# Optimization experiments

Measured on AMD Instinct MI355X. Metric: run time of the kernel, lower is better.

## Reference

```python
import jax, jax.numpy as jnp
import numpy as np

N_NODES = 50000
N_EDGES = 800000
IN_F, H_F, OUT_F = 256, 256, 128


def setup_inputs() -> dict:
    key = jax.random.key(0)
    k1, k2, k3, k4, k5, k6 = jax.random.split(key, 6)
    in_feat = jax.random.normal(k1, (N_NODES, IN_F), dtype=jnp.float32)
    src = jax.random.randint(k2, (N_EDGES,), 0, N_NODES, dtype=jnp.int32)
    dst = jax.random.randint(k3, (N_EDGES,), 0, N_NODES, dtype=jnp.int32)
    s1 = 1.0 / np.sqrt(IN_F)
    s2 = 1.0 / np.sqrt(H_F)
    W1 = jax.random.uniform(k4, (IN_F, H_F), dtype=jnp.float32, minval=-s1, maxval=s1)
    b1 = jnp.zeros((H_F,), dtype=jnp.float32)
    W2 = jax.random.uniform(k5, (H_F, OUT_F), dtype=jnp.float32, minval=-s2, maxval=s2)
    b2 = jnp.zeros((OUT_F,), dtype=jnp.float32)
    return {"in_feat": in_feat, "src": src, "dst": dst,
            "W1": W1, "b1": b1, "W2": W2, "b2": b2}


def _graph_conv(x, W, b, src, dst, n_nodes):
    # DGL GraphConv with norm='both':
    #   h = D_in^{-1/2} A D_out^{-1/2} (X W) + b   (degrees clamped to min 1)
    ones = jnp.ones((src.shape[0],), dtype=x.dtype)
    deg_out = jax.ops.segment_sum(ones, src, num_segments=n_nodes)
    deg_in = jax.ops.segment_sum(ones, dst, num_segments=n_nodes)
    norm_out = jax.lax.rsqrt(jnp.maximum(deg_out, 1.0))  # [N]
    norm_in = jax.lax.rsqrt(jnp.maximum(deg_in, 1.0))    # [N]
    h = (x @ W) * norm_out[:, None]                       # [N, F_out]
    agg = jax.ops.segment_sum(h[src], dst, num_segments=n_nodes)  # SpMM
    return agg * norm_in[:, None] + b


def reference(in_feat, src, dst, W1, b1, W2, b2):
    n = in_feat.shape[0]
    h = _graph_conv(in_feat, W1, b1, src, dst, n)
    h = jax.nn.relu(h)
    h = _graph_conv(h, W2, b2, src, dst, n)
    # dgl.mean_nodes over a single graph -> mean across all nodes
    return jnp.mean(h, axis=0)  # [OUT_F]
```

## Files before the change

### kernel.cpp

```cpp
#include <hip/hip_runtime.h>


#define NNODES 50000
#define NEDGES 800000
#define DPAD   32
#define G1_BM   ((NNODES + 127) / 128)
#define MEGA_NB 3911
#define WS_NB   2048
#define NQUAD   (NNODES / 4)

typedef __bf16 bf16x8 __attribute__((ext_vector_type(8)));
typedef float f32x4 __attribute__((ext_vector_type(4)));
typedef float f32x2 __attribute__((ext_vector_type(2)));

__device__ __forceinline__ unsigned short f2b(float f) {
    union { float f; unsigned u; } v; v.f = f;
    unsigned r = 0x7fffu + ((v.u >> 16) & 1u);
    return (unsigned short)((v.u + r) >> 16);
}
__device__ __forceinline__ unsigned char f2fp8(float x) {
    return (unsigned char)(__builtin_amdgcn_cvt_pk_fp8_f32(x, x, 0, false) & 0xff);
}
__device__ __forceinline__ float rdeg(int d) {
    return __frsqrt_rn((float)max(d, 1));
}

__global__ void k_cast_w1(const float* __restrict__ W1, unsigned short* __restrict__ W1t,
                          uint4* __restrict__ deg0) {
    int id = blockIdx.x * blockDim.x + threadIdx.x;
    int k = id >> 8, n = id & 255;
    W1t[n * 256 + k] = f2b(W1[id]);
    const uint4 z = make_uint4(0, 0, 0, 0);
    for (int j = id; j < 2 * NNODES * DPAD / 4; j += 65536) deg0[j] = z;
}

__global__ __launch_bounds__(256) void k_mega1(
    const int* __restrict__ src, const int* __restrict__ dst,
    int* __restrict__ degOut, int* __restrict__ degIn,
    unsigned short* __restrict__ col2, unsigned short* __restrict__ dst2,
    const float* __restrict__ X, const unsigned short* __restrict__ W1t,
    unsigned char* __restrict__ H, int M) {
    __shared__ __align__(16) unsigned short As[128][40];
    __shared__ __align__(16) unsigned short Bs[128][40];

    int bid = blockIdx.x;
    int tid = threadIdx.x;

    if ((bid % 5) != 4) {
        int did = bid - (bid + 1) / 5;
        int e = did * 256 + tid;
        if (e < NEDGES) {
            int s = src[e], d = dst[e];
            int si = atomicAdd(&degIn[d * DPAD], 1);
            if (si < 64) col2[d * 64 + si] = (unsigned short)s;
            int so = atomicAdd(&degOut[s * DPAD], 1);
            if (so < 64) dst2[s * 64 + so] = (unsigned short)d;
        }
        return;
    }

    int g = bid / 5;
    int bm = g % G1_BM, bn = g / G1_BM;
    int m0 = bm * 128, n0 = bn * 128;
    int lane = tid & 63, wave = tid >> 6;
    int wm = (wave >> 1) * 64, wn = (wave & 1) * 64;
    int q = lane >> 4, r16 = lane & 15;

    f32x4 acc[4][4];
#pragma unroll
    for (int i = 0; i < 4; i++)
#pragma unroll
        for (int j = 0; j < 4; j++) acc[i][j] = 0.f;

    int c0 = tid, c1 = tid + 256;
    int r0 = c0 >> 2, k0c = (c0 & 3) * 8;
    int r1 = c1 >> 2, k1c = (c1 & 3) * 8;
    const float* Ar0 = X + (size_t)min(m0 + r0, M - 1) * 256;
    const float* Ar1 = X + (size_t)min(m0 + r1, M - 1) * 256;
    const unsigned short* Br0 = W1t + (size_t)(n0 + r0) * 256;
    const unsigned short* Br1 = W1t + (size_t)(n0 + r1) * 256;

    auto pk2u = [](float a, float b) -> unsigned {
        unsigned short x = f2b(a), y = f2b(b);
        return (unsigned)x | ((unsigned)y << 16);
    };

    for (int k0 = 0; k0 < 256; k0 += 32) {
        float4 fa0 = *(const float4*)(Ar0 + k0 + k0c);
        float4 fa1 = *(const float4*)(Ar0 + k0 + k0c + 4);
        float4 fb0 = *(const float4*)(Ar1 + k0 + k1c);
        float4 fb1 = *(const float4*)(Ar1 + k0 + k1c + 4);
        uint4 vb0 = *(const uint4*)(Br0 + k0 + k0c);
        uint4 vb1 = *(const uint4*)(Br1 + k0 + k1c);
        uint4 va0 = make_uint4(pk2u(fa0.x, fa0.y), pk2u(fa0.z, fa0.w), pk2u(fa1.x, fa1.y), pk2u(fa1.z, fa1.w));
        uint4 va1 = make_uint4(pk2u(fb0.x, fb0.y), pk2u(fb0.z, fb0.w), pk2u(fb1.x, fb1.y), pk2u(fb1.z, fb1.w));
        __syncthreads();
        *(uint4*)&As[r0][k0c] = va0;
        *(uint4*)&As[r1][k1c] = va1;
        *(uint4*)&Bs[r0][k0c] = vb0;
        *(uint4*)&Bs[r1][k1c] = vb1;
        __syncthreads();
        bf16x8 af[4], bf[4];
#pragma unroll
        for (int i = 0; i < 4; i++)
            af[i] = *(const bf16x8*)&As[wm + i * 16 + r16][q * 8];
#pragma unroll
        for (int j = 0; j < 4; j++)
            bf[j] = *(const bf16x8*)&Bs[wn + j * 16 + r16][q * 8];
#pragma unroll
        for (int i = 0; i < 4; i++)
#pragma unroll
            for (int j = 0; j < 4; j++)
                acc[i][j] = __builtin_amdgcn_mfma_f32_16x16x32_bf16(af[i], bf[j], acc[i][j], 0, 0, 0);
    }

#pragma unroll
    for (int i = 0; i < 4; i++) {
#pragma unroll
        for (int rr = 0; rr < 4; rr++) {
            int m = m0 + wm + i * 16 + q * 4 + rr;
            if (m < M) {
                unsigned char* Hp = H + (size_t)m * 256 + n0 + wn + r16;
#pragma unroll
                for (int j = 0; j < 4; j++)
                    Hp[j * 16] = f2fp8(acc[i][j][rr]);
            }
        }
    }
}

__global__ __launch_bounds__(256) void k_norms(
    const int* __restrict__ degOut, const int* __restrict__ degIn,
    float* __restrict__ normOut, float* __restrict__ normIn,
    int* __restrict__ degc) {
    int i = blockIdx.x * blockDim.x + threadIdx.x;
    if (i < NNODES) {
        int dI = degIn[i * DPAD], dO = degOut[i * DPAD];
        normIn[i] = rdeg(dI);
        normOut[i] = rdeg(dO);
        degc[i] = min(dI, 64) | (min(dO, 64) << 16);
    }
}

__global__ __launch_bounds__(256) void k_spmm_wsum(
    const unsigned char* __restrict__ H, const float* __restrict__ normIn,
    const float* __restrict__ normOut, const int* __restrict__ degc,
    const unsigned short* __restrict__ col2, const unsigned short* __restrict__ dst2,
    const float* __restrict__ bias, float* __restrict__ vpart) {
    __shared__ float sm[4][256];
    int wave = threadIdx.x >> 6;
    int lane = threadIdx.x & 63;
    int f = lane * 4;
    const unsigned char* Hf = H + f;
    float4 bv = *(const float4*)(bias + f);
    float vac0 = 0.f, vac1 = 0.f, vac2 = 0.f, vac3 = 0.f;

    int qd = blockIdx.x;
    int node = qd * 4 + wave;
    int pDC = 0, pc = 0, pd = 0;
    float pNI = 0.f, pNO = 0.f;
    if (qd < NQUAD) {
        pDC = degc[node]; pNI = normIn[node]; pNO = normOut[node];
        pc = (int)col2[(size_t)node * 64 + lane];
        pd = (int)dst2[(size_t)node * 64 + lane];
    }

    while (qd < NQUAD) {
        int dI = pDC & 0xffff, dO = pDC >> 16;
        float nI = pNI, nO = pNO;
        int myc = pc, myd = pd;

        int nqd = qd + gridDim.x;
        if (nqd < NQUAD) {
            int nn = nqd * 4 + wave;
            pDC = degc[nn]; pNI = normIn[nn]; pNO = normOut[nn];
            pc = (int)col2[(size_t)nn * 64 + lane];
            pd = (int)dst2[(size_t)nn * 64 + lane];
        }

        float sIn = 0.f;
        if (lane < dO) sIn = normIn[myd];
#pragma unroll
        for (int o = 32; o > 0; o >>= 1) sIn += __shfl_xor(sIn, o);
        float wn = nO * sIn;

        float a0 = 0.f, a1 = 0.f, a2 = 0.f, a3 = 0.f;
        int i = 0;
        for (; i + 16 <= dI; i += 16) {
            float w[16]; unsigned v[16];
#pragma unroll
            for (int u = 0; u < 16; u++) {
                int c = __builtin_amdgcn_readlane(myc, i + u);
                w[u] = normOut[c];
                v[u] = *(const unsigned*)(Hf + (size_t)c * 256);
            }
#pragma unroll
            for (int u = 0; u < 16; u++) {
                f32x2 lo = __builtin_amdgcn_cvt_pk_f32_fp8(v[u], false);
                f32x2 hi = __builtin_amdgcn_cvt_pk_f32_fp8(v[u], true);
                a0 += lo.x * w[u]; a1 += lo.y * w[u];
                a2 += hi.x * w[u]; a3 += hi.y * w[u];
            }
        }
        for (; i + 4 <= dI; i += 4) {
            float w[4]; unsigned v[4];
#pragma unroll
            for (int u = 0; u < 4; u++) {
                int c = __builtin_amdgcn_readlane(myc, i + u);
                w[u] = normOut[c];
                v[u] = *(const unsigned*)(Hf + (size_t)c * 256);
            }
#pragma unroll
            for (int u = 0; u < 4; u++) {
                f32x2 lo = __builtin_amdgcn_cvt_pk_f32_fp8(v[u], false);
                f32x2 hi = __builtin_amdgcn_cvt_pk_f32_fp8(v[u], true);
                a0 += lo.x * w[u]; a1 += lo.y * w[u];
                a2 += hi.x * w[u]; a3 += hi.y * w[u];
            }
        }
        for (; i < dI; i++) {
            int c = __builtin_amdgcn_readlane(myc, i);
            float w = normOut[c];
            unsigned v = *(const unsigned*)(Hf + (size_t)c * 256);
            f32x2 lo = __builtin_amdgcn_cvt_pk_f32_fp8(v, false);
            f32x2 hi = __builtin_amdgcn_cvt_pk_f32_fp8(v, true);
            a0 += lo.x * w; a1 += lo.y * w;
            a2 += hi.x * w; a3 += hi.y * w;
        }

        vac0 += wn * fmaxf(a0 * nI + bv.x, 0.f);
        vac1 += wn * fmaxf(a1 * nI + bv.y, 0.f);
        vac2 += wn * fmaxf(a2 * nI + bv.z, 0.f);
        vac3 += wn * fmaxf(a3 * nI + bv.w, 0.f);

        qd = nqd;
    }

    *(float4*)&sm[wave][f] = make_float4(vac0, vac1, vac2, vac3);
    __syncthreads();
    int t = threadIdx.x;
    float s4 = sm[0][t] + sm[1][t] + sm[2][t] + sm[3][t];
    vpart[(size_t)blockIdx.x * 256 + t] = s4;
}

__global__ __launch_bounds__(256) void k_red1(const float* __restrict__ vpart,
                                              float* __restrict__ vred) {
    int b = blockIdx.x;
    int t = threadIdx.x;
    float s = 0.f;
    for (int i = b; i < WS_NB; i += 64) s += vpart[(size_t)i * 256 + t];
    vred[(size_t)b * 256 + t] = s;
}

__global__ __launch_bounds__(1024) void k_final(
    const float* __restrict__ vred, const float* __restrict__ W2,
    const float* __restrict__ b2, float* __restrict__ out) {
    __shared__ float part[4][256];
    __shared__ float v[256];
    int t = threadIdx.x;
    int feat = t & 255, pr = t >> 8;
    float s = 0.f;
    for (int i = pr; i < 64; i += 4) s += vred[(size_t)i * 256 + feat];
    part[pr][feat] = s;
    __syncthreads();
    if (t < 256) v[t] = part[0][t] + part[1][t] + part[2][t] + part[3][t];
    __syncthreads();
    if (t < 128) {
        float o = 0.f;
        for (int k = 0; k < 256; k++) o += v[k] * W2[k * 128 + t];
        out[t] = o * (1.0f / (float)NNODES) + b2[t];
    }
}

extern "C" void kernel_launch(void* const* d_in, const int* in_sizes, int n_in,
                              void* d_out, int out_size, void* d_ws, size_t ws_size,
                              hipStream_t stream) {
    const float* X   = (const float*)d_in[0];
    const int*   src = (const int*)d_in[1];
    const int*   dst = (const int*)d_in[2];
    const float* W1  = (const float*)d_in[3];
    const float* b1  = (const float*)d_in[4];
    const float* W2  = (const float*)d_in[5];
    const float* b2  = (const float*)d_in[6];
    float* out = (float*)d_out;

    const int n = NNODES;

    char* p = (char*)d_ws;
    auto carve = [&](size_t bytes) -> void* {
        void* r = (void*)p;
        p += (bytes + 255) & ~(size_t)255;
        return r;
    };
    int*   degOut  = (int*)carve((size_t)2 * n * DPAD * sizeof(int));
    int*   degIn   = degOut + (size_t)n * DPAD;
    unsigned short* col2 = (unsigned short*)carve((size_t)n * 64 * 2);
    unsigned short* dst2 = (unsigned short*)carve((size_t)n * 64 * 2);
    unsigned short* W1t  = (unsigned short*)carve((size_t)256 * 256 * 2);
    unsigned char*  bufA = (unsigned char*)carve((size_t)n * 256);
    float* vpart  = (float*)carve((size_t)WS_NB * 256 * sizeof(float));
    float* vred   = (float*)carve((size_t)64 * 256 * sizeof(float));
    float* normOutD = (float*)carve((size_t)n * sizeof(float));
    float* normInD  = (float*)carve((size_t)n * sizeof(float));
    int*   degc     = (int*)carve((size_t)n * sizeof(int));

    k_cast_w1<<<256, 256, 0, stream>>>(W1, W1t, (uint4*)degOut);

    k_mega1<<<MEGA_NB, 256, 0, stream>>>(src, dst, degOut, degIn, col2, dst2, X, W1t, bufA, n);

    k_norms<<<(n + 255) / 256, 256, 0, stream>>>(degOut, degIn, normOutD, normInD, degc);

    k_spmm_wsum<<<WS_NB, 256, 0, stream>>>(bufA, normInD, normOutD, degc, col2, dst2, b1, vpart);

    k_red1<<<64, 256, 0, stream>>>(vpart, vred);
    k_final<<<1, 1024, 0, stream>>>(vred, W2, b2, out);
}
```

Measured before the change: 230.2 us.

## Replace out-degree CSR with LDS histograms for out-degree and weight sums

Drops the per-source adjacency (dst2) and padded out-degree atomics from the edge pass. A new histogram kernel computes out-degree and the per-source sum of normIn[dst] in shared-memory partial sums over edge chunks, and a merge kernel reduces them into norms and a precomputed weight per node. The SpMM kernel then reads that weight instead of gathering normIn over dst2 and doing a wave reduction. The cost is an extra full edge pass plus large partial-sum scratch traffic, in exchange for fewer global atomics and scattered writes. DegIn padding is also removed, so in-degree atomics now hit adjacent words.

```diff
diff --git a/kernel.cpp b/kernel.cpp
--- a/kernel.cpp
+++ b/kernel.cpp
@@ -3,11 +3,14 @@
 
 #define NNODES 50000
 #define NEDGES 800000
-#define DPAD   32
 #define G1_BM   ((NNODES + 127) / 128)
 #define MEGA_NB 3911
 #define WS_NB   2048
 #define NQUAD   (NNODES / 4)
+#define CH      64
+#define EPC     (NEDGES / CH)
+#define QN      12500
+#define HN      25000
 
 typedef __bf16 bf16x8 __attribute__((ext_vector_type(8)));
 typedef float f32x4 __attribute__((ext_vector_type(4)));
@@ -30,14 +33,12 @@
     int id = blockIdx.x * blockDim.x + threadIdx.x;
     int k = id >> 8, n = id & 255;
     W1t[n * 256 + k] = f2b(W1[id]);
-    const uint4 z = make_uint4(0, 0, 0, 0);
-    for (int j = id; j < 2 * NNODES * DPAD / 4; j += 65536) deg0[j] = z;
+    if (id < NNODES / 4) deg0[id] = make_uint4(0, 0, 0, 0);
 }
 
 __global__ __launch_bounds__(256) void k_mega1(
     const int* __restrict__ src, const int* __restrict__ dst,
-    int* __restrict__ degOut, int* __restrict__ degIn,
-    unsigned short* __restrict__ col2, unsigned short* __restrict__ dst2,
+    int* __restrict__ degIn, unsigned short* __restrict__ col2,
     const float* __restrict__ X, const unsigned short* __restrict__ W1t,
     unsigned char* __restrict__ H, int M) {
     __shared__ __align__(16) unsigned short As[128][40];
@@ -51,10 +52,8 @@
         int e = did * 256 + tid;
         if (e < NEDGES) {
             int s = src[e], d = dst[e];
-            int si = atomicAdd(&degIn[d * DPAD], 1);
+            int si = atomicAdd(&degIn[d], 1);
             if (si < 64) col2[d * 64 + si] = (unsigned short)s;
-            int so = atomicAdd(&degOut[s * DPAD], 1);
-            if (so < 64) dst2[s * 64 + so] = (unsigned short)d;
         }
         return;
     }
@@ -129,23 +128,77 @@
     }
 }
 
-__global__ __launch_bounds__(256) void k_norms(
-    const int* __restrict__ degOut, const int* __restrict__ degIn,
-    float* __restrict__ normOut, float* __restrict__ normIn,
-    int* __restrict__ degc) {
+__global__ __launch_bounds__(256) void k_hist(
+    const int* __restrict__ src, const int* __restrict__ dst,
+    const int* __restrict__ degIn,
+    float* __restrict__ wsumP,
+    unsigned* __restrict__ degOutP)
+{
+    __shared__ unsigned lds[QN];
+    int b = blockIdx.x, t = threadIdx.x;
+    for (int i = t; i < QN; i += 256) lds[i] = 0;
+    __syncthreads();
+
+    if (b < 256) {
+        int c = b >> 2, q = b & 3;
+        int base = c * EPC;
+        int lo = q * QN;
+        float* w = (float*)lds;
+        for (int e = base + t; e < base + EPC; e += 256) {
+            int s = src[e], d = dst[e];
+            unsigned r = (unsigned)(s - lo);
+            if (r < QN) {
+                float ni = rdeg(degIn[d]);
+                atomicAdd(&w[r], ni);
+            }
+        }
+        __syncthreads();
+        float* outp = wsumP + (size_t)b * QN;
+        for (int i = t; i < QN; i += 256) outp[i] = w[i];
+    } else {
+        int b2 = b - 256;
+        int c = b2 >> 1, h = b2 & 1;
+        int base = c * EPC;
+        int lo = h * HN;
+        for (int e = base + t; e < base + EPC; e += 256) {
+            unsigned r = (unsigned)(src[e] - lo);
+            if (r < HN) atomicAdd(&lds[r >> 1], 1u << ((r & 1) * 16));
+        }
+        __syncthreads();
+        unsigned* outp = degOutP + (size_t)b2 * QN;
+        for (int i = t; i < QN; i += 256) outp[i] = lds[i];
+    }
+}
+
+__global__ __launch_bounds__(256) void k_merge(
+    const float* __restrict__ wsumP, const unsigned* __restrict__ degOutP,
+    const int* __restrict__ degIn,
+    float* __restrict__ normIn, float* __restrict__ normOut,
+    float* __restrict__ wgt, int* __restrict__ degc) {
     int i = blockIdx.x * blockDim.x + threadIdx.x;
-    if (i < NNODES) {
-        int dI = degIn[i * DPAD], dO = degOut[i * DPAD];
-        normIn[i] = rdeg(dI);
-        normOut[i] = rdeg(dO);
-        degc[i] = min(dI, 64) | (min(dO, 64) << 16);
-    }
+    if (i >= NNODES) return;
+    int q = i / QN, li = i - q * QN;
+    float ws = 0.f;
+#pragma unroll 8
+    for (int c = 0; c < CH; c++) ws += wsumP[(size_t)(c * 4 + q) * QN + li];
+    int h = i / HN, r = i - h * HN;
+    int wd = r >> 1, sel = r & 1;
+    unsigned dsum = 0;
+#pragma unroll 8
+    for (int c = 0; c < CH; c++) dsum += degOutP[(size_t)(c * 2 + h) * QN + wd];
+    int dO = (int)((dsum >> (sel * 16)) & 0xffffu);
+    int dI = degIn[i];
+    float nI = rdeg(dI), nO = rdeg(dO);
+    normIn[i] = nI;
+    normOut[i] = nO;
+    wgt[i] = nO * ws;
+    degc[i] = min(dI, 64);
 }
 
 __global__ __launch_bounds__(256) void k_spmm_wsum(
     const unsigned char* __restrict__ H, const float* __restrict__ normIn,
-    const float* __restrict__ normOut, const int* __restrict__ degc,
-    const unsigned short* __restrict__ col2, const unsigned short* __restrict__ dst2,
+    const float* __restrict__ normOut, const float* __restrict__ wgt,
+    const int* __restrict__ degc, const unsigned short* __restrict__ col2,
     const float* __restrict__ bias, float* __restrict__ vpart) {
     __shared__ float sm[4][256];
     int wave = threadIdx.x >> 6;
@@ -157,32 +210,23 @@
 
     int qd = blockIdx.x;
     int node = qd * 4 + wave;
-    int pDC = 0, pc = 0, pd = 0;
-    float pNI = 0.f, pNO = 0.f;
+    int pDI = 0, pc = 0;
+    float pNI = 0.f, pW = 0.f;
     if (qd < NQUAD) {
-        pDC = degc[node]; pNI = normIn[node]; pNO = normOut[node];
+        pDI = degc[node]; pNI = normIn[node]; pW = wgt[node];
         pc = (int)col2[(size_t)node * 64 + lane];
-        pd = (int)dst2[(size_t)node * 64 + lane];
     }
 
     while (qd < NQUAD) {
-        int dI = pDC & 0xffff, dO = pDC >> 16;
-        float nI = pNI, nO = pNO;
-        int myc = pc, myd = pd;
+        int dI = pDI, myc = pc;
+        float nI = pNI, wn = pW;
 
         int nqd = qd + gridDim.x;
         if (nqd < NQUAD) {
             int nn = nqd * 4 + wave;
-            pDC = degc[nn]; pNI = normIn[nn]; pNO = normOut[nn];
+            pDI = degc[nn]; pNI = normIn[nn]; pW = wgt[nn];
             pc = (int)col2[(size_t)nn * 64 + lane];
-            pd = (int)dst2[(size_t)nn * 64 + lane];
-        }
-
-        float sIn = 0.f;
-        if (lane < dO) sIn = normIn[myd];
-#pragma unroll
-        for (int o = 32; o > 0; o >>= 1) sIn += __shfl_xor(sIn, o);
-        float wn = nO * sIn;
+        }
 
         float a0 = 0.f, a1 = 0.f, a2 = 0.f, a3 = 0.f;
         int i = 0;
@@ -292,25 +336,32 @@
         p += (bytes + 255) & ~(size_t)255;
         return r;
     };
-    int*   degOut  = (int*)carve((size_t)2 * n * DPAD * sizeof(int));
-    int*   degIn   = degOut + (size_t)n * DPAD;
+    int*   degIn   = (int*)carve((size_t)n * sizeof(int));
     unsigned short* col2 = (unsigned short*)carve((size_t)n * 64 * 2);
-    unsigned short* dst2 = (unsigned short*)carve((size_t)n * 64 * 2);
     unsigned short* W1t  = (unsigned short*)carve((size_t)256 * 256 * 2);
     unsigned char*  bufA = (unsigned char*)carve((size_t)n * 256);
-    float* vpart  = (float*)carve((size_t)WS_NB * 256 * sizeof(float));
-    float* vred   = (float*)carve((size_t)64 * 256 * sizeof(float));
-    float* normOutD = (float*)carve((size_t)n * sizeof(float));
-    float* normInD  = (float*)carve((size_t)n * sizeof(float));
-    int*   degc     = (int*)carve((size_t)n * sizeof(int));
-
-    k_cast_w1<<<256, 256, 0, stream>>>(W1, W1t, (uint4*)degOut);
-
-    k_mega1<<<MEGA_NB, 256, 0, stream>>>(src, dst, degOut, degIn, col2, dst2, X, W1t, bufA, n);
-
-    k_norms<<<(n + 255) / 256, 256, 0, stream>>>(degOut, degIn, normOutD, normInD, degc);
-
-    k_spmm_wsum<<<WS_NB, 256, 0, stream>>>(bufA, normInD, normOutD, degc, col2, dst2, b1, vpart);
+    float* normIn  = (float*)carve((size_t)n * sizeof(float));
+    float* normOut = (float*)carve((size_t)n * sizeof(float));
+    float* wgt     = (float*)carve((size_t)n * sizeof(float));
+    int*   degc    = (int*)carve((size_t)n * sizeof(int));
+    size_t wsumP_bytes   = (size_t)256 * QN * sizeof(float);
+    size_t degOutP_bytes = (size_t)128 * QN * sizeof(unsigned);
+    char* scratch = (char*)carve(wsumP_bytes + degOutP_bytes);
+    float*    wsumP   = (float*)scratch;
+    unsigned* degOutP = (unsigned*)(scratch + wsumP_bytes);
+    float* vpart = (float*)scratch;
+    float* vred  = (float*)(scratch + (size_t)WS_NB * 256 * sizeof(float));
+
+    k_cast_w1<<<256, 256, 0, stream>>>(W1, W1t, (uint4*)degIn);
+
+    k_mega1<<<MEGA_NB, 256, 0, stream>>>(src, dst, degIn, col2, X, W1t, bufA, n);
+
+    k_hist<<<384, 256, 0, stream>>>(src, dst, degIn, wsumP, degOutP);
+
+    k_merge<<<(n + 255) / 256, 256, 0, stream>>>(wsumP, degOutP, degIn,
+                                                 normIn, normOut, wgt, degc);
+
+    k_spmm_wsum<<<WS_NB, 256, 0, stream>>>(bufA, normIn, normOut, wgt, degc, col2, b1, vpart);
 
     k_red1<<<64, 256, 0, stream>>>(vpart, vred);
     k_final<<<1, 1024, 0, stream>>>(vred, W2, b2, out);
```

Result: slower. 234.9 us (+2.1%).
